# Kernel optimization log

Measured on AMD Instinct MI355X. Metric: run time of the kernel, lower is better.

Reference implementation:

```python
import jax, jax.numpy as jnp
import numpy as np
from jax import lax

B, INP, OUP, H, W = 16, 128, 128, 56, 56
EXPAND = 6
HID = INP * EXPAND  # 768
EPS = 1e-5


def setup_inputs() -> dict:
    key = jax.random.key(0)
    ks = jax.random.split(key, 18)
    x = jax.random.normal(ks[0], (B, INP, H, W), dtype=jnp.float32)
    mask = jax.random.randint(ks[1], (B, 1, H, W), 0, 2, dtype=jnp.int32)
    w1 = jax.random.normal(ks[2], (HID, INP), dtype=jnp.float32) * 0.05
    g1 = 1.0 + 0.1 * jax.random.normal(ks[3], (HID,), dtype=jnp.float32)
    b1 = 0.1 * jax.random.normal(ks[4], (HID,), dtype=jnp.float32)
    m1 = 0.1 * jax.random.normal(ks[5], (HID,), dtype=jnp.float32)
    v1 = jax.random.uniform(ks[6], (HID,), dtype=jnp.float32) + 0.5
    wdw = jax.random.normal(ks[7], (HID, 1, 3, 3), dtype=jnp.float32) * 0.05
    g2 = 1.0 + 0.1 * jax.random.normal(ks[8], (HID,), dtype=jnp.float32)
    b2 = 0.1 * jax.random.normal(ks[9], (HID,), dtype=jnp.float32)
    m2 = 0.1 * jax.random.normal(ks[10], (HID,), dtype=jnp.float32)
    v2 = jax.random.uniform(ks[11], (HID,), dtype=jnp.float32) + 0.5
    w2 = jax.random.normal(ks[12], (OUP, HID), dtype=jnp.float32) * 0.05
    g3 = 1.0 + 0.1 * jax.random.normal(ks[13], (OUP,), dtype=jnp.float32)
    b3 = 0.1 * jax.random.normal(ks[14], (OUP,), dtype=jnp.float32)
    m3 = 0.1 * jax.random.normal(ks[15], (OUP,), dtype=jnp.float32)
    v3 = jax.random.uniform(ks[16], (OUP,), dtype=jnp.float32) + 0.5
    return dict(x=x, w1=w1, g1=g1, b1=b1, m1=m1, v1=v1, wdw=wdw,
                g2=g2, b2=b2, m2=m2, v2=v2, w2=w2,
                g3=g3, b3=b3, m3=m3, v3=v3, mask=mask)


def _bn(h, g, b, m, v):
    # inference-mode BatchNorm2d: (h - mean) * gamma/sqrt(var+eps) + beta
    scale = g / jnp.sqrt(v + EPS)
    return (h - m[None, :, None, None]) * scale[None, :, None, None] + b[None, :, None, None]


def reference(x, w1, g1, b1, m1, v1, wdw, g2, b2, m2, v2, w2, g3, b3, m3, v3, mask):
    mf = mask.astype(x.dtype)  # [B,1,H,W] binary mask ('std')
    # mask_dilate: 3x3 binary dilation (dilate_stride=1) so the depthwise conv
    # has valid neighbors for every active output pixel
    md = lax.reduce_window(mf, 0.0, lax.max, (1, 1, 3, 3), (1, 1, 1, 1), 'SAME')
    # expand 1x1 conv + BN + ReLU6, restricted to dilated mask
    h = jnp.einsum('bchw,kc->bkhw', x, w1)            # [B,HID,H,W]
    h = jnp.clip(_bn(h, g1, b1, m1, v1), 0.0, 6.0) * md
    # depthwise 3x3 conv + BN + ReLU6, restricted to std mask
    h = lax.conv_general_dilated(h, wdw, (1, 1), 'SAME',
                                 feature_group_count=HID,
                                 dimension_numbers=('NCHW', 'OIHW', 'NCHW'))
    h = jnp.clip(_bn(h, g2, b2, m2, v2), 0.0, 6.0) * mf
    # project 1x1 conv + BN (no relu), restricted to std mask
    h = jnp.einsum('bkhw,ok->bohw', h, w2)            # [B,OUP,H,W]
    h = _bn(h, g3, b3, m3, v3) * mf
    # scatter-add into identity path
    return x + h
```

## Files before the change

### kernel.cpp

```cpp
#include <hip/hip_runtime.h>
#include <hip/hip_bf16.h>

#define BATCH 16
#define INP   128
#define OUP   128
#define HH    56
#define WW    56
#define HWSZ  3136
#define HID   768
#define EPSV  1e-5f

#define SCPD  62
#define ROWD  (32 * SCPD)
#define H2STR 72

typedef __attribute__((ext_vector_type(8))) short bf16x8;
typedef __attribute__((ext_vector_type(4))) float f32x4;

__device__ __forceinline__ unsigned short f2b(float f) {
    unsigned u = __float_as_uint(f);
    return (unsigned short)((u + 0x7FFFu + ((u >> 16) & 1u)) >> 16);
}
__device__ __forceinline__ unsigned pkbf(float lo, float hi) {
    unsigned r;
    asm("v_cvt_pk_bf16_f32 %0, %1, %2" : "=v"(r) : "v"(lo), "v"(hi));
    return r;
}

__global__ void prep(const float* __restrict__ w1, const float* __restrict__ g1,
                     const float* __restrict__ b1, const float* __restrict__ m1, const float* __restrict__ v1,
                     const float* __restrict__ wdw, const float* __restrict__ g2,
                     const float* __restrict__ b2, const float* __restrict__ m2, const float* __restrict__ v2,
                     const float* __restrict__ w2, const float* __restrict__ g3,
                     const float* __restrict__ b3, const float* __restrict__ m3, const float* __restrict__ v3,
                     const int* __restrict__ mask,
                     unsigned short* __restrict__ w1f, unsigned short* __restrict__ w2f,
                     float* __restrict__ be1o, float* __restrict__ wdsf,
                     float* __restrict__ be2o, float* __restrict__ be3o,
                     float* __restrict__ mdf, float* __restrict__ mff)
{
    int gid = blockIdx.x * blockDim.x + threadIdx.x;
    int stp = gridDim.x * blockDim.x;
    for (int i = gid; i < HID * INP; i += stp) {
        int r = i >> 7, k = i & 127;
        float s = g1[r] * rsqrtf(v1[r] + EPSV);
        int ht = r >> 4, r16 = r & 15, ks = k >> 5, g = (k >> 3) & 3, e = k & 7;
        w1f[((((ht * 4 + ks) * 4 + g) * 16 + r16) << 3) + e] = f2b(w1[i] * s);
    }
    for (int i = gid; i < OUP * HID; i += stp) {
        int r = i / HID, k = i - r * HID;
        float s = g3[r] * rsqrtf(v3[r] + EPSV);
        int ot = r >> 4, r16 = r & 15, ch = k >> 6, ks = (k >> 5) & 1, g = (k >> 3) & 3, e = k & 7;
        int lane = g * 16 + r16;
        w2f[((((ot * 12 + ch) * 2 + ks) * 64 + lane) << 3) + e] = f2b(w2[i] * s);
    }
    for (int i = gid; i < HID; i += stp) {
        float s1 = g1[i] * rsqrtf(v1[i] + EPSV);
        be1o[i] = b1[i] - m1[i] * s1;
        float s2 = g2[i] * rsqrtf(v2[i] + EPSV);
        be2o[i] = b2[i] - m2[i] * s2;
    }
    for (int i = gid; i < HID * 9; i += stp) {
        int q = i / HID, c = i - q * HID;
        float s2 = g2[c] * rsqrtf(v2[c] + EPSV);
        wdsf[i] = wdw[c * 9 + q] * s2;
    }
    for (int i = gid; i < OUP; i += stp) {
        float s3 = g3[i] * rsqrtf(v3[i] + EPSV);
        be3o[i] = b3[i] - m3[i] * s3;
    }
    for (int i = gid; i < BATCH * HWSZ; i += stp) {
        int b = i / HWSZ, p = i - b * HWSZ;
        int y = p / WW, xx = p - y * WW;
        float mf = (float)mask[i];
        float md = 0.f;
        for (int dy = -1; dy <= 1; ++dy)
            for (int dx = -1; dx <= 1; ++dx) {
                int yy = y + dy, xc = xx + dx;
                if (yy >= 0 && yy < HH && xc >= 0 && xc < WW)
                    md = fmaxf(md, (float)mask[b * HWSZ + yy * WW + xc]);
            }
        mff[i] = mf;
        mdf[i] = md;
    }
}

__launch_bounds__(512, 4)
__global__ void k1_expand(const float* __restrict__ x,
                          const unsigned short* __restrict__ w1f,
                          const float* __restrict__ be1g,
                          const float* __restrict__ mdf,
                          unsigned* __restrict__ h1p)
{
    __shared__ unsigned short xs[128 * 128];
    const int t = threadIdx.x, lane = t & 63, wv = t >> 6;
    const int g = lane >> 4, r16 = lane & 15;
    const int pid = blockIdx.x;
    const int l = (pid & 7) * 150 + (pid >> 3);
    const int hb = l % 3;
    const int pb = (l / 3) % 25;
    const int b  = l / 75;
    const int p0 = pb * 128;
    const int whid = wv & 3;
    const int wpx  = wv >> 2;

    for (int rep = 0; rep < 8; ++rep) {
        int id = t + rep * 512;
        int px = id & 127, c4 = id >> 7;
        int p = p0 + px;
        ushort4 u; u.x = 0; u.y = 0; u.z = 0; u.w = 0;
        if (p < HWSZ) {
            const float* xp = x + ((size_t)(b * INP + c4 * 4)) * HWSZ + p;
            unsigned lo = pkbf(xp[0], xp[HWSZ]);
            unsigned hi = pkbf(xp[2 * HWSZ], xp[3 * HWSZ]);
            u.x = (unsigned short)lo; u.y = (unsigned short)(lo >> 16);
            u.z = (unsigned short)hi; u.w = (unsigned short)(hi >> 16);
        }
        *(ushort4*)&xs[px * 128 + (((c4 >> 1) ^ (px & 15)) << 3) + ((c4 & 1) << 2)] = u;
    }
    __syncthreads();

    f32x4 acc[4][4];
    #pragma unroll
    for (int mt = 0; mt < 4; ++mt)
        #pragma unroll
        for (int nt = 0; nt < 4; ++nt) {
            acc[mt][nt][0] = 0.f; acc[mt][nt][1] = 0.f;
            acc[mt][nt][2] = 0.f; acc[mt][nt][3] = 0.f;
        }
    const int hbase = hb * 256 + whid * 64;
    const int htb = hbase >> 4;

    #pragma unroll
    for (int ks = 0; ks < 4; ++ks) {
        bf16x8 af[4];
        #pragma unroll
        for (int mt = 0; mt < 4; ++mt)
            af[mt] = *(const bf16x8*)&w1f[((((htb + mt) * 4 + ks) * 64) + lane) << 3];
        #pragma unroll
        for (int nt = 0; nt < 4; ++nt) {
            int px = wpx * 64 + nt * 16 + r16;
            bf16x8 bf = *(const bf16x8*)&xs[px * 128 + (((ks * 4 + g) ^ r16) << 3)];
            #pragma unroll
            for (int mt = 0; mt < 4; ++mt)
                acc[mt][nt] = __builtin_amdgcn_mfma_f32_16x16x32_bf16(af[mt], bf, acc[mt][nt], 0, 0, 0);
        }
    }

    #pragma unroll
    for (int nt = 0; nt < 4; ++nt) {
        const int pg = p0 + wpx * 64 + nt * 16;
        if (pg >= HWSZ) continue;
        const int p = pg + r16;
        const float md = mdf[b * HWSZ + p];
        #pragma unroll
        for (int mt = 0; mt < 4; ++mt) {
            const float4 be4 = *(const float4*)&be1g[hbase + mt * 16 + g * 4];
            f32x4 a = acc[mt][nt];
            float v0 = fminf(fmaxf(a[0] + be4.x, 0.f), 6.f) * md;
            float v1 = fminf(fmaxf(a[1] + be4.y, 0.f), 6.f) * md;
            float v2 = fminf(fmaxf(a[2] + be4.z, 0.f), 6.f) * md;
            float v3 = fminf(fmaxf(a[3] + be4.w, 0.f), 6.f) * md;
            const int c2 = (hbase >> 1) + mt * 8 + g * 2;
            const size_t ad = (size_t)(b * 384 + c2) * HWSZ + p;
            h1p[ad] = pkbf(v0, v1);
            h1p[ad + HWSZ] = pkbf(v2, v3);
        }
    }
}

__launch_bounds__(512, 4)
__global__ void k23(const unsigned* __restrict__ h1p,
                    const unsigned short* __restrict__ w2f,
                    const float* __restrict__ wdsf,
                    const float* __restrict__ be2g,
                    const float* __restrict__ be3g,
                    const float* __restrict__ mff,
                    const float* __restrict__ x,
                    float* __restrict__ out)
{
    __shared__ unsigned stg[2 * 4 * ROWD];
    __shared__ unsigned short h2s[112 * H2STR];
    __shared__ float mfv_[112];

    const int t = threadIdx.x, lane = t & 63, wv = t >> 6;
    const int g = lane >> 4, r16 = lane & 15;
    const int pid = blockIdx.x;
    const int l = (pid & 7) * 56 + (pid >> 3);
    const int strip = l % 28, b = l / 28;
    const int y0 = strip * 2, p0 = strip * 112;

    if (t < 112) mfv_[t] = mff[b * HWSZ + p0 + t];
    {
        int cp = t & 31, rs = (t >> 5) & 7, side = t >> 8;
        stg[rs * ROWD + cp * SCPD + (side ? 58 : 1)] = 0;
    }

    auto stage = [&](int ch) {
        #pragma unroll
        for (int rep = 0; rep < 4; ++rep) {
            const int id = t + rep * 512;
            if (id < 1792) {
                const int rr  = (id * 4682) >> 16;
                const int px4 = id - rr * 14;
                const int row = rr & 3, cp = rr >> 2;
                const int gy = y0 - 1 + row;
                uint4 u; u.x = 0; u.y = 0; u.z = 0; u.w = 0;
                if (gy >= 0 && gy < HH)
                    u = *(const uint4*)&h1p[(size_t)(b * 384 + ch * 32 + cp) * HWSZ + gy * WW + px4 * 4];
                unsigned* s = &stg[((ch & 1) * 4 + row) * ROWD + cp * SCPD + 2 + px4 * 4];
                uint2 a; a.x = u.x; a.y = u.y;
                uint2 c; c.x = u.z; c.y = u.w;
                *(uint2*)(s) = a;
                *(uint2*)(s + 2) = c;
            }
        }
    };

    const int c = lane, row2 = (t >> 6) & 1, q = t >> 7;
    const int cp_dw = c >> 1;
    const int shl = (c & 1) ? 0 : 16;

    auto phaseDW = [&](int ch) {
        float wt[9];
        #pragma unroll
        for (int q9 = 0; q9 < 9; ++q9) wt[q9] = wdsf[q9 * HID + ch * 64 + c];
        const float be = be2g[ch * 64 + c];
        float acc[14];
        #pragma unroll
        for (int j = 0; j < 14; ++j) acc[j] = be;
        const unsigned* sb = &stg[(ch & 1) * 4 * ROWD + cp_dw * SCPD + 2 + q * 14];
        #pragma unroll
        for (int dy = 0; dy < 3; ++dy) {
            const unsigned* rp = sb + (row2 + dy) * ROWD;
            unsigned uw[16];
            uw[0] = rp[-1];
            #pragma unroll
            for (int i = 0; i < 7; ++i) {
                uint2 d = *(const uint2*)(rp + 2 * i);
                uw[1 + 2 * i] = d.x; uw[2 + 2 * i] = d.y;
            }
            uw[15] = rp[14];
            float fl[16];
            #pragma unroll
            for (int i = 0; i < 16; ++i)
                fl[i] = __uint_as_float((uw[i] << shl) & 0xFFFF0000u);
            #pragma unroll
            for (int j = 0; j < 14; ++j)
                acc[j] += fl[j] * wt[dy * 3] + fl[j + 1] * wt[dy * 3 + 1] + fl[j + 2] * wt[dy * 3 + 2];
        }
        #pragma unroll
        for (int j = 0; j < 14; ++j) {
            const int px = row2 * 56 + q * 14 + j;
            const float mv = mfv_[px];
            float v = fminf(fmaxf(acc[j], 0.f), 6.f) * mv;
            h2s[px * H2STR + (((c >> 3) ^ (px & 7)) << 3) + (c & 7)] = (unsigned short)pkbf(v, v);
        }
    };

    f32x4 pacc[7];
    #pragma unroll
    for (int nt = 0; nt < 7; ++nt) {
        pacc[nt][0] = 0.f; pacc[nt][1] = 0.f; pacc[nt][2] = 0.f; pacc[nt][3] = 0.f;
    }

    auto phaseP = [&](int ch) {
        #pragma unroll
        for (int ks = 0; ks < 2; ++ks) {
            const bf16x8 pw = *(const bf16x8*)&w2f[((((wv * 12 + ch) * 2 + ks) * 64) + lane) << 3];
            #pragma unroll
            for (int nt = 0; nt < 7; ++nt) {
                const int px = nt * 16 + r16;
                const bf16x8 hb = *(const bf16x8*)&h2s[px * H2STR + (((ks * 4 + g) ^ (px & 7)) << 3)];
                pacc[nt] = __builtin_amdgcn_mfma_f32_16x16x32_bf16(pw, hb, pacc[nt], 0, 0, 0);
            }
        }
    };

    stage(0);
    __syncthreads();
    for (int ch = 0; ch < 12; ++ch) {
        phaseDW(ch);
        __syncthreads();
        if (ch + 1 < 12) stage(ch + 1);
        phaseP(ch);
        __syncthreads();
    }

    {
        const int ob = wv * 16 + g * 4;
        const float4 be4 = *(const float4*)&be3g[ob];
        #pragma unroll
        for (int nt = 0; nt < 7; ++nt) {
            const int px = nt * 16 + r16;
            const float mv = mfv_[px];
            const size_t base = (size_t)(b * OUP + ob) * HWSZ + p0 + px;
            out[base]            = x[base]            + (pacc[nt][0] + be4.x) * mv;
            out[base + HWSZ]     = x[base + HWSZ]     + (pacc[nt][1] + be4.y) * mv;
            out[base + 2 * HWSZ] = x[base + 2 * HWSZ] + (pacc[nt][2] + be4.z) * mv;
            out[base + 3 * HWSZ] = x[base + 3 * HWSZ] + (pacc[nt][3] + be4.w) * mv;
        }
    }
}

extern "C" void kernel_launch(void* const* d_in, const int* in_sizes, int n_in,
                              void* d_out, int out_size, void* d_ws, size_t ws_size,
                              hipStream_t stream) {
    (void)in_sizes; (void)n_in; (void)out_size; (void)ws_size;
    const float* x   = (const float*)d_in[0];
    const float* w1  = (const float*)d_in[1];
    const float* g1  = (const float*)d_in[2];
    const float* b1  = (const float*)d_in[3];
    const float* m1  = (const float*)d_in[4];
    const float* v1  = (const float*)d_in[5];
    const float* wdw = (const float*)d_in[6];
    const float* g2  = (const float*)d_in[7];
    const float* b2  = (const float*)d_in[8];
    const float* m2  = (const float*)d_in[9];
    const float* v2  = (const float*)d_in[10];
    const float* w2  = (const float*)d_in[11];
    const float* g3  = (const float*)d_in[12];
    const float* b3  = (const float*)d_in[13];
    const float* m3  = (const float*)d_in[14];
    const float* v3  = (const float*)d_in[15];
    const int*  mask = (const int*)d_in[16];
    float* out = (float*)d_out;

    char* ws = (char*)d_ws;
    unsigned short* w1f = (unsigned short*)ws;
    unsigned short* w2f = (unsigned short*)(ws + 196608);
    float* be1o = (float*)(ws + 393216);
    float* wdsf = (float*)(ws + 396288);
    float* be2o = (float*)(ws + 423936);
    float* be3o = (float*)(ws + 427008);
    float* mdf  = (float*)(ws + 427520);
    float* mff  = (float*)(ws + 628224);
    unsigned* h1p = (unsigned*)(ws + 828928);

    prep<<<256, 256, 0, stream>>>(w1, g1, b1, m1, v1, wdw, g2, b2, m2, v2,
                                  w2, g3, b3, m3, v3, mask,
                                  w1f, w2f, be1o, wdsf, be2o, be3o, mdf, mff);
    k1_expand<<<dim3(1200), 512, 0, stream>>>(x, w1f, be1o, mdf, h1p);
    k23<<<dim3(448), 512, 0, stream>>>(h1p, w2f, wdsf, be2o, be3o, mff, x, out);
}
```

Measured before the change: 92.78 us.

## Single-buffer DW staging with register prefetch and skip masked depthwise pixels

The double-buffered LDS staging becomes a single buffer. The next channel group's global loads are issued into registers before the depthwise phase and written to LDS after the barrier, with the address math precomputed once. The depthwise conv now keeps the three input rows in registers and skips the 9-tap sum for pixels whose mask is zero, using a wave-uniform readfirstlane test because the mask is per pixel and shared across the wave's channels. Cutting LDS allows a higher occupancy hint (6 blocks per launch bound) and a larger h2s stride, at the cost of more live registers for the prefetched data.

```diff
diff --git a/kernel.cpp b/kernel.cpp
--- a/kernel.cpp
+++ b/kernel.cpp
@@ -12,7 +12,7 @@
 
 #define SCPD  62
 #define ROWD  (32 * SCPD)
-#define H2STR 72
+#define H2STR 80
 
 typedef __attribute__((ext_vector_type(8))) short bf16x8;
 typedef __attribute__((ext_vector_type(4))) float f32x4;
@@ -169,7 +169,7 @@
     }
 }
 
-__launch_bounds__(512, 4)
+__launch_bounds__(512, 6)
 __global__ void k23(const unsigned* __restrict__ h1p,
                     const unsigned short* __restrict__ w2f,
                     const float* __restrict__ wdsf,
@@ -179,7 +179,7 @@
                     const float* __restrict__ x,
                     float* __restrict__ out)
 {
-    __shared__ unsigned stg[2 * 4 * ROWD];
+    __shared__ unsigned stg[4 * ROWD];
     __shared__ unsigned short h2s[112 * H2STR];
     __shared__ float mfv_[112];
 
@@ -191,26 +191,42 @@
     const int y0 = strip * 2, p0 = strip * 112;
 
     if (t < 112) mfv_[t] = mff[b * HWSZ + p0 + t];
-    {
-        int cp = t & 31, rs = (t >> 5) & 7, side = t >> 8;
+    if (t < 256) {
+        int cp = t & 31, rs = (t >> 5) & 3, side = t >> 7;
         stg[rs * ROWD + cp * SCPD + (side ? 58 : 1)] = 0;
     }
 
-    auto stage = [&](int ch) {
+    unsigned gaddr[4]; int laddr[4]; bool gval[4], wval[4];
+    #pragma unroll
+    for (int rep = 0; rep < 4; ++rep) {
+        const int id = t + rep * 512;
+        const int rr  = (id * 4682) >> 16;
+        const int px4 = id - rr * 14;
+        const int row = rr & 3, cp = rr >> 2;
+        const int gy = y0 - 1 + row;
+        wval[rep] = id < 1792;
+        gval[rep] = wval[rep] && gy >= 0 && gy < HH;
+        gaddr[rep] = (unsigned)((b * 384 + cp) * HWSZ + gy * WW + px4 * 4);
+        laddr[rep] = row * ROWD + cp * SCPD + 2 + px4 * 4;
+    }
+    uint4 sreg[4];
+
+    auto issueLoads = [&]() {
         #pragma unroll
         for (int rep = 0; rep < 4; ++rep) {
-            const int id = t + rep * 512;
-            if (id < 1792) {
-                const int rr  = (id * 4682) >> 16;
-                const int px4 = id - rr * 14;
-                const int row = rr & 3, cp = rr >> 2;
-                const int gy = y0 - 1 + row;
-                uint4 u; u.x = 0; u.y = 0; u.z = 0; u.w = 0;
-                if (gy >= 0 && gy < HH)
-                    u = *(const uint4*)&h1p[(size_t)(b * 384 + ch * 32 + cp) * HWSZ + gy * WW + px4 * 4];
-                unsigned* s = &stg[((ch & 1) * 4 + row) * ROWD + cp * SCPD + 2 + px4 * 4];
-                uint2 a; a.x = u.x; a.y = u.y;
-                uint2 c; c.x = u.z; c.y = u.w;
+            uint4 u; u.x = 0; u.y = 0; u.z = 0; u.w = 0;
+            if (gval[rep]) u = *(const uint4*)&h1p[gaddr[rep]];
+            sreg[rep] = u;
+            gaddr[rep] += 32 * HWSZ;
+        }
+    };
+    auto stageWrite = [&]() {
+        #pragma unroll
+        for (int rep = 0; rep < 4; ++rep) {
+            if (wval[rep]) {
+                unsigned* s = &stg[laddr[rep]];
+                uint2 a; a.x = sreg[rep].x; a.y = sreg[rep].y;
+                uint2 c; c.x = sreg[rep].z; c.y = sreg[rep].w;
                 *(uint2*)(s) = a;
                 *(uint2*)(s + 2) = c;
             }
@@ -220,19 +236,18 @@
     const int c = lane, row2 = (t >> 6) & 1, q = t >> 7;
     const int cp_dw = c >> 1;
     const int shl = (c & 1) ? 0 : 16;
+    const unsigned* dwbase = &stg[cp_dw * SCPD + 2 + q * 14];
+    unsigned short* h2wr = &h2s[(c & 7) + (((c >> 3)) << 3)];
 
     auto phaseDW = [&](int ch) {
         float wt[9];
         #pragma unroll
         for (int q9 = 0; q9 < 9; ++q9) wt[q9] = wdsf[q9 * HID + ch * 64 + c];
         const float be = be2g[ch * 64 + c];
-        float acc[14];
-        #pragma unroll
-        for (int j = 0; j < 14; ++j) acc[j] = be;
-        const unsigned* sb = &stg[(ch & 1) * 4 * ROWD + cp_dw * SCPD + 2 + q * 14];
+        float rr_[3][16];
         #pragma unroll
         for (int dy = 0; dy < 3; ++dy) {
-            const unsigned* rp = sb + (row2 + dy) * ROWD;
+            const unsigned* rp = dwbase + (row2 + dy) * ROWD;
             unsigned uw[16];
             uw[0] = rp[-1];
             #pragma unroll
@@ -241,20 +256,23 @@
                 uw[1 + 2 * i] = d.x; uw[2 + 2 * i] = d.y;
             }
             uw[15] = rp[14];
-            float fl[16];
             #pragma unroll
             for (int i = 0; i < 16; ++i)
-                fl[i] = __uint_as_float((uw[i] << shl) & 0xFFFF0000u);
-            #pragma unroll
-            for (int j = 0; j < 14; ++j)
-                acc[j] += fl[j] * wt[dy * 3] + fl[j + 1] * wt[dy * 3 + 1] + fl[j + 2] * wt[dy * 3 + 2];
+                rr_[dy][i] = __uint_as_float((uw[i] << shl) & 0xFFFF0000u);
         }
         #pragma unroll
         for (int j = 0; j < 14; ++j) {
             const int px = row2 * 56 + q * 14 + j;
             const float mv = mfv_[px];
-            float v = fminf(fmaxf(acc[j], 0.f), 6.f) * mv;
-            h2s[px * H2STR + (((c >> 3) ^ (px & 7)) << 3) + (c & 7)] = (unsigned short)pkbf(v, v);
+            unsigned short hv = 0;
+            if (__builtin_amdgcn_readfirstlane(__float_as_uint(mv)) != 0) {
+                float s = rr_[0][j] * wt[0] + rr_[0][j + 1] * wt[1] + rr_[0][j + 2] * wt[2]
+                        + rr_[1][j] * wt[3] + rr_[1][j + 1] * wt[4] + rr_[1][j + 2] * wt[5]
+                        + rr_[2][j] * wt[6] + rr_[2][j + 1] * wt[7] + rr_[2][j + 2] * wt[8];
+                float v = fminf(fmaxf(s + be, 0.f), 6.f);
+                hv = (unsigned short)pkbf(v, v);
+            }
+            h2s[px * H2STR + (((c >> 3) ^ (px & 7)) << 3) + (c & 7)] = hv;
         }
     };
 
@@ -277,12 +295,14 @@
         }
     };
 
-    stage(0);
+    issueLoads();
+    stageWrite();
     __syncthreads();
     for (int ch = 0; ch < 12; ++ch) {
+        if (ch + 1 < 12) issueLoads();
         phaseDW(ch);
         __syncthreads();
-        if (ch + 1 < 12) stage(ch + 1);
+        if (ch + 1 < 12) stageWrite();
         phaseP(ch);
         __syncthreads();
     }
```

New measurement: 271.8 us. 2.93x slower.
